# Performance work log

Measured on AMD Instinct MI355X. Metric: run time of the kernel, lower is better.

Reference implementation:

```python
import jax, jax.numpy as jnp
import numpy as np

V, E, H = 32000, 128, 128

def setup_inputs() -> dict:
    key = jax.random.key(0)
    ks = jax.random.split(key, 12)
    s = 0.05
    x = jax.random.randint(ks[0], (256, 512), 0, V)
    emb = jax.random.normal(ks[1], (V, E), jnp.float32) * s
    Wi = jax.random.normal(ks[2], (E + H, H), jnp.float32) * s
    bi = jnp.zeros((H,), jnp.float32)
    Wf = jax.random.normal(ks[3], (E + H, H), jnp.float32) * s
    bf = jnp.zeros((H,), jnp.float32)
    Wc = jax.random.normal(ks[4], (E + H, H), jnp.float32) * s
    bc = jnp.zeros((H,), jnp.float32)
    Wo = jax.random.normal(ks[5], (E + H, H), jnp.float32) * s
    bo = jnp.zeros((H,), jnp.float32)
    Wout = jax.random.normal(ks[6], (H, V), jnp.float32) * s
    bout = jnp.zeros((V,), jnp.float32)
    return {"x": x, "emb": emb, "Wi": Wi, "bi": bi, "Wf": Wf, "bf": bf,
            "Wc": Wc, "bc": bc, "Wo": Wo, "bo": bo, "Wout": Wout, "bout": bout}

def reference(x, emb, Wi, bi, Wf, bf, Wc, bc, Wo, bo, Wout, bout):
    B, T = x.shape
    xe = emb[x]                       # [B, T, E] embedding gather
    xe_t = jnp.swapaxes(xe, 0, 1)     # [T, B, E] for scan over time

    def step(carry, e_t):
        h, c = carry
        comb = jnp.concatenate([e_t, h], axis=1)          # [B, E+H]
        f = jax.nn.sigmoid(comb @ Wf + bf)
        i = jax.nn.sigmoid(comb @ Wi + bi)
        o = jax.nn.sigmoid(comb @ Wo + bo)
        c_ = jnp.tanh(comb @ Wc + bc)
        c = f * c + i * c_
        h = o * jnp.tanh(c)
        return (h, c), None

    h0 = jnp.zeros((B, H), xe.dtype)
    c0 = jnp.zeros((B, H), xe.dtype)
    (h, _), _ = jax.lax.scan(step, (h0, c0), xe_t)
    return h @ Wout + bout            # [B, V] logits from final hidden state
```

## Files before the change

kernel.cpp:

```cpp
#include <hip/hip_runtime.h>

constexpr int TT = 512;
constexpr int BB = 256;
constexpr int HH = 128;
constexpr int VV = 32000;

typedef _Float16 h2 __attribute__((ext_vector_type(2)));
typedef _Float16 f16x4 __attribute__((ext_vector_type(4)));
typedef _Float16 f16x8 __attribute__((ext_vector_type(8)));
typedef float f32x4 __attribute__((ext_vector_type(4)));

struct __align__(16) H2x4 { h2 a, b, c, d; };

__device__ __forceinline__ h2 pkrtz(float a, float b) {
  return __builtin_bit_cast(h2, __builtin_amdgcn_cvt_pkrtz(a, b));
}
__device__ __forceinline__ float fexp2(float x) {
  return __builtin_amdgcn_exp2f(x);
}
__device__ __forceinline__ float frcp(float x) {
  return __builtin_amdgcn_rcpf(x);
}
__device__ __forceinline__ float fdot2(h2 a, h2 b, float c) {
  return __builtin_amdgcn_fdot2(a, b, c, false);
}
template <int CTRL>
__device__ __forceinline__ float qmov(float v) {
  return __builtin_bit_cast(
      float, __builtin_amdgcn_mov_dpp(__builtin_bit_cast(int, v), CTRL, 0xf,
                                      0xf, true));
}

constexpr float SC_SIG = -1.4426950408889634f;
constexpr float SC_TANH = 2.8853900817779268f;

__global__ __launch_bounds__(256, 4) void wprep(
    const float* __restrict__ Wi, const float* __restrict__ bi,
    const float* __restrict__ Wf, const float* __restrict__ bf,
    const float* __restrict__ Wc, const float* __restrict__ bc,
    const float* __restrict__ Wo, const float* __restrict__ bo,
    _Float16* __restrict__ Wct, float* __restrict__ bcat) {
  const int n = blockIdx.x;
  const int g = n & 3;
  const int u = n >> 2;
  const float* Wg = (g == 0) ? Wi : (g == 1) ? Wf : (g == 2) ? Wc : Wo;
  const float* bg = (g == 0) ? bi : (g == 1) ? bf : (g == 2) ? bc : bo;
  const float sc = (g == 2) ? SC_TANH : SC_SIG;
  const int k = threadIdx.x;
  Wct[(size_t)n * 256 + k] = (_Float16)(Wg[(size_t)k * HH + u] * sc);
  if (k == 0) bcat[n] = bg[u] * sc;
}

__global__ __launch_bounds__(512, 2) void lstm_rec(
    const int* __restrict__ x, const float* __restrict__ emb,
    const _Float16* __restrict__ Wct, const float* __restrict__ bcat,
    _Float16* __restrict__ hbf) {
  const int b = blockIdx.x;
  const int tid = threadIdx.x;
  const int g = tid & 3;
  const int u = tid >> 2;
  const int w = tid >> 6;
  const int l = tid & 63;
  const int n16 = l & 15;
  const int quad = l >> 4;

  __shared__ int xrow[TT];
  __shared__ __align__(16) _Float16 comb[2][HH];
  __shared__ __align__(16) _Float16 xch[64][516];

  xrow[tid] = x[(size_t)b * TT + tid];
  if (tid < HH) comb[0][tid] = (_Float16)0.f;

  h2 wh2[64];
  {
    const _Float16* wp = Wct + (size_t)tid * 256 + 128;
#pragma unroll
    for (int j = 0; j < 16; ++j) {
      const H2x4 q = __builtin_bit_cast(H2x4, *(const f16x8*)(wp + 8 * j));
      wh2[4 * j + 0] = q.a;
      wh2[4 * j + 1] = q.b;
      wh2[4 * j + 2] = q.c;
      wh2[4 * j + 3] = q.d;
    }
  }

  f16x8 wfx[4][4];
  f32x4 biasr[4];
#pragma unroll
  for (int nt = 0; nt < 4; ++nt) {
#pragma unroll
    for (int ks = 0; ks < 4; ++ks)
      wfx[nt][ks] = *(const f16x8*)(Wct +
                                    (size_t)(64 * w + nt * 16 + n16) * 256 +
                                    ks * 32 + quad * 8);
    biasr[nt] = *(const f32x4*)(bcat + 64 * w + nt * 16 + quad * 4);
  }

  const float gam = (g == 2) ? -2.f : 1.f;
  const float del = (g == 2) ? 1.f : 0.f;

  const f32x4 ZR4 = {0.f, 0.f, 0.f, 0.f};

  float cst = 0.f;
  float hv = 0.f;
  int buf = 0;

  __syncthreads();

  for (int c = 0; c < 8; ++c) {
#pragma unroll 2
    for (int tt = 0; tt < 4; ++tt) {
      const int vid = xrow[c * 64 + tt * 16 + n16];
      const float* ep = emb + (size_t)vid * HH + quad * 8;
      f16x8 ef[4];
#pragma unroll
      for (int ks = 0; ks < 4; ++ks) {
        const float4 e0 = *(const float4*)(ep + ks * 32);
        const float4 e1 = *(const float4*)(ep + ks * 32 + 4);
        H2x4 q;
        q.a = pkrtz(e0.x, e0.y);
        q.b = pkrtz(e0.z, e0.w);
        q.c = pkrtz(e1.x, e1.y);
        q.d = pkrtz(e1.z, e1.w);
        ef[ks] = __builtin_bit_cast(f16x8, q);
      }
      f32x4 acc[4];
#pragma unroll
      for (int nt = 0; nt < 4; ++nt)
        acc[nt] = __builtin_amdgcn_mfma_f32_16x16x32_f16(wfx[nt][0], ef[0],
                                                         ZR4, 0, 0, 0);
#pragma unroll
      for (int ks = 1; ks < 4; ++ks)
#pragma unroll
        for (int nt = 0; nt < 4; ++nt)
          acc[nt] = __builtin_amdgcn_mfma_f32_16x16x32_f16(wfx[nt][ks], ef[ks],
                                                           acc[nt], 0, 0, 0);
#pragma unroll
      for (int nt = 0; nt < 4; ++nt) {
        const f32x4 av = acc[nt] + biasr[nt];
        _Float16* dst = &xch[tt * 16 + n16][64 * w + nt * 16 + quad * 4];
        *(h2*)dst = pkrtz(av[0], av[1]);
        *(h2*)(dst + 2) = pkrtz(av[2], av[3]);
      }
    }
    __syncthreads();

#pragma unroll 2
    for (int tl = 0; tl < 64; ++tl) {
      const float xe = (float)xch[tl][tid];

      const _Float16* cb = comb[buf];
      float s0 = 0.f, s1 = 0.f, s2 = 0.f, s3 = 0.f;
#pragma unroll
      for (int j = 0; j < 16; ++j) {
        const H2x4 hq = __builtin_bit_cast(H2x4, *(const f16x8*)(cb + 8 * j));
        s0 = fdot2(hq.a, wh2[4 * j + 0], s0);
        s1 = fdot2(hq.b, wh2[4 * j + 1], s1);
        s2 = fdot2(hq.c, wh2[4 * j + 2], s2);
        s3 = fdot2(hq.d, wh2[4 * j + 3], s3);
      }
      const float a = (s0 + s1) + (s2 + s3) + xe;

      const float act = gam * frcp(1.f + fexp2(a)) + del;

      const float x1 = qmov<0xB1>(act);
      const float x2 = qmov<0x4E>(act);
      const float x3 = qmov<0x4E>(x1);

      cst = x1 * cst + act * x2;
      const float th = 1.f - 2.f * frcp(1.f + fexp2(cst * SC_TANH));
      hv = x3 * th;

      if (g == 0) comb[buf ^ 1][u] = (_Float16)hv;
      __syncthreads();
      buf ^= 1;
    }
  }
  if (g == 0) hbf[(size_t)b * HH + u] = (_Float16)hv;
}

__global__ __launch_bounds__(256, 4) void wout_tr(const float* __restrict__ Wout,
                                                  _Float16* __restrict__ Wt) {
  const int v = blockIdx.x * 256 + threadIdx.x;
#pragma unroll 1
  for (int kc = 0; kc < 16; ++kc) {
    float f[8];
#pragma unroll
    for (int i = 0; i < 8; ++i) f[i] = Wout[(size_t)(kc * 8 + i) * VV + v];
    H2x4 q;
    q.a = pkrtz(f[0], f[1]);
    q.b = pkrtz(f[2], f[3]);
    q.c = pkrtz(f[4], f[5]);
    q.d = pkrtz(f[6], f[7]);
    *(H2x4*)(Wt + (size_t)v * HH + kc * 8) = q;
  }
}

__global__ __launch_bounds__(256, 4) void lstm_out(
    const _Float16* __restrict__ Wt, const _Float16* __restrict__ hbf,
    const float* __restrict__ bout, float* __restrict__ out) {
  const int tid = threadIdx.x;
  const int wv = tid >> 6;
  const int lane = tid & 63;
  const int vblk = blockIdx.x % 250;
  const int batblk = blockIdx.x / 250;
  const int n16 = lane & 15;
  const int quad = lane >> 4;
  const int vbase = vblk * 128 + wv * 32;
  const int batbase = batblk * 64;

  f32x4 acc[4][2] = {};
#pragma unroll
  for (int ks = 0; ks < 4; ++ks) {
    const int k = ks * 32 + quad * 8;
    f16x8 a[4], bf_[2];
#pragma unroll
    for (int mt = 0; mt < 4; ++mt)
      a[mt] = *(const f16x8*)(hbf + (size_t)(batbase + mt * 16 + n16) * HH + k);
#pragma unroll
    for (int vt = 0; vt < 2; ++vt)
      bf_[vt] = *(const f16x8*)(Wt + (size_t)(vbase + vt * 16 + n16) * HH + k);
#pragma unroll
    for (int mt = 0; mt < 4; ++mt)
#pragma unroll
      for (int vt = 0; vt < 2; ++vt)
        acc[mt][vt] = __builtin_amdgcn_mfma_f32_16x16x32_f16(a[mt], bf_[vt],
                                                             acc[mt][vt], 0, 0, 0);
  }
#pragma unroll
  for (int vt = 0; vt < 2; ++vt) {
    const int v = vbase + vt * 16 + n16;
    const float bv = bout[v];
#pragma unroll
    for (int mt = 0; mt < 4; ++mt) {
#pragma unroll
      for (int r = 0; r < 4; ++r) {
        const int bat = batbase + mt * 16 + quad * 4 + r;
        out[(size_t)bat * VV + v] = acc[mt][vt][r] + bv;
      }
    }
  }
}

extern "C" void kernel_launch(void* const* d_in, const int* in_sizes, int n_in,
                              void* d_out, int out_size, void* d_ws,
                              size_t ws_size, hipStream_t stream) {
  const int* x = (const int*)d_in[0];
  const float* emb = (const float*)d_in[1];
  const float* Wi = (const float*)d_in[2];
  const float* bi = (const float*)d_in[3];
  const float* Wf = (const float*)d_in[4];
  const float* bf = (const float*)d_in[5];
  const float* Wc = (const float*)d_in[6];
  const float* bc = (const float*)d_in[7];
  const float* Wo = (const float*)d_in[8];
  const float* bo = (const float*)d_in[9];
  const float* Wout = (const float*)d_in[10];
  const float* bout = (const float*)d_in[11];
  float* out = (float*)d_out;

  _Float16* Wt = (_Float16*)d_ws;
  _Float16* hbf = Wt + (size_t)VV * HH;
  _Float16* Wct = hbf + (size_t)BB * HH;
  float* bcat = (float*)(Wct + 512 * 256);

  wprep<<<512, 256, 0, stream>>>(Wi, bi, Wf, bf, Wc, bc, Wo, bo, Wct, bcat);
  wout_tr<<<VV / 256, 256, 0, stream>>>(Wout, Wt);
  lstm_rec<<<BB, 512, 0, stream>>>(x, emb, Wct, bcat, hbf);
  lstm_out<<<(VV / 128) * (BB / 64), 256, 0, stream>>>(Wt, hbf, bout, out);
}
```

Measured before the change: 439.7 us.

## Split recurrent dot product across two lanes with 1024-thread blocks

Doubles the recurrence block to 1024 threads, so each gate row's hidden-state dot product is split over two lanes (64 elements each) and combined with a ds_swizzle xor-4 exchange. The input-projection MFMA weights are no longer kept in registers; they are loaded from global memory on each tile, and each wave now handles 32 gate rows instead of 64. This halves the serial fdot2 chain and the weight registers per thread, shortening the per-timestep critical path. In exchange it adds a cross-lane swizzle and a 1024-thread barrier on every step, plus repeated global weight loads in the projection phase.

```diff
diff --git a/kernel.cpp b/kernel.cpp
--- a/kernel.cpp
+++ b/kernel.cpp
@@ -29,6 +29,10 @@
   return __builtin_bit_cast(
       float, __builtin_amdgcn_mov_dpp(__builtin_bit_cast(int, v), CTRL, 0xf,
                                       0xf, true));
+}
+__device__ __forceinline__ float swz_xor4(float v) {
+  return __builtin_bit_cast(
+      float, __builtin_amdgcn_ds_swizzle(__builtin_bit_cast(int, v), 0x101F));
 }
 
 constexpr float SC_SIG = -1.4426950408889634f;
@@ -51,31 +55,34 @@
   if (k == 0) bcat[n] = bg[u] * sc;
 }
 
-__global__ __launch_bounds__(512, 2) void lstm_rec(
+__global__ __launch_bounds__(1024, 4) void lstm_rec(
     const int* __restrict__ x, const float* __restrict__ emb,
     const _Float16* __restrict__ Wct, const float* __restrict__ bcat,
     _Float16* __restrict__ hbf) {
   const int b = blockIdx.x;
   const int tid = threadIdx.x;
-  const int g = tid & 3;
-  const int u = tid >> 2;
   const int w = tid >> 6;
   const int l = tid & 63;
   const int n16 = l & 15;
   const int quad = l >> 4;
+  const int g = l & 3;
+  const int kh = (l >> 2) & 1;
+  const int uloc = l >> 3;
+  const int u = 8 * w + uloc;
+  const int n = 32 * w + 4 * uloc + g;
 
   __shared__ int xrow[TT];
   __shared__ __align__(16) _Float16 comb[2][HH];
   __shared__ __align__(16) _Float16 xch[64][516];
 
-  xrow[tid] = x[(size_t)b * TT + tid];
+  if (tid < TT) xrow[tid] = x[(size_t)b * TT + tid];
   if (tid < HH) comb[0][tid] = (_Float16)0.f;
 
-  h2 wh2[64];
+  h2 wh2[32];
   {
-    const _Float16* wp = Wct + (size_t)tid * 256 + 128;
-#pragma unroll
-    for (int j = 0; j < 16; ++j) {
+    const _Float16* wp = Wct + (size_t)n * 256 + 128 + 64 * kh;
+#pragma unroll
+    for (int j = 0; j < 8; ++j) {
       const H2x4 q = __builtin_bit_cast(H2x4, *(const f16x8*)(wp + 8 * j));
       wh2[4 * j + 0] = q.a;
       wh2[4 * j + 1] = q.b;
@@ -84,18 +91,6 @@
     }
   }
 
-  f16x8 wfx[4][4];
-  f32x4 biasr[4];
-#pragma unroll
-  for (int nt = 0; nt < 4; ++nt) {
-#pragma unroll
-    for (int ks = 0; ks < 4; ++ks)
-      wfx[nt][ks] = *(const f16x8*)(Wct +
-                                    (size_t)(64 * w + nt * 16 + n16) * 256 +
-                                    ks * 32 + quad * 8);
-    biasr[nt] = *(const f32x4*)(bcat + 64 * w + nt * 16 + quad * 4);
-  }
-
   const float gam = (g == 2) ? -2.f : 1.f;
   const float del = (g == 2) ? 1.f : 0.f;
 
@@ -108,7 +103,7 @@
   __syncthreads();
 
   for (int c = 0; c < 8; ++c) {
-#pragma unroll 2
+#pragma unroll 1
     for (int tt = 0; tt < 4; ++tt) {
       const int vid = xrow[c * 64 + tt * 16 + n16];
       const float* ep = emb + (size_t)vid * HH + quad * 8;
@@ -124,21 +119,19 @@
         q.d = pkrtz(e1.z, e1.w);
         ef[ks] = __builtin_bit_cast(f16x8, q);
       }
-      f32x4 acc[4];
-#pragma unroll
-      for (int nt = 0; nt < 4; ++nt)
-        acc[nt] = __builtin_amdgcn_mfma_f32_16x16x32_f16(wfx[nt][0], ef[0],
-                                                         ZR4, 0, 0, 0);
-#pragma unroll
-      for (int ks = 1; ks < 4; ++ks)
-#pragma unroll
-        for (int nt = 0; nt < 4; ++nt)
-          acc[nt] = __builtin_amdgcn_mfma_f32_16x16x32_f16(wfx[nt][ks], ef[ks],
-                                                           acc[nt], 0, 0, 0);
-#pragma unroll
-      for (int nt = 0; nt < 4; ++nt) {
-        const f32x4 av = acc[nt] + biasr[nt];
-        _Float16* dst = &xch[tt * 16 + n16][64 * w + nt * 16 + quad * 4];
+#pragma unroll
+      for (int nt = 0; nt < 2; ++nt) {
+        const _Float16* wbase = Wct + (size_t)(32 * w + nt * 16 + n16) * 256;
+        f32x4 acc = __builtin_amdgcn_mfma_f32_16x16x32_f16(
+            *(const f16x8*)(wbase + 0 * 32 + quad * 8), ef[0], ZR4, 0, 0, 0);
+#pragma unroll
+        for (int ks = 1; ks < 4; ++ks)
+          acc = __builtin_amdgcn_mfma_f32_16x16x32_f16(
+              *(const f16x8*)(wbase + ks * 32 + quad * 8), ef[ks], acc, 0, 0,
+              0);
+        const f32x4 av =
+            acc + *(const f32x4*)(bcat + 32 * w + nt * 16 + quad * 4);
+        _Float16* dst = &xch[tt * 16 + n16][32 * w + nt * 16 + quad * 4];
         *(h2*)dst = pkrtz(av[0], av[1]);
         *(h2*)(dst + 2) = pkrtz(av[2], av[3]);
       }
@@ -147,19 +140,20 @@
 
 #pragma unroll 2
     for (int tl = 0; tl < 64; ++tl) {
-      const float xe = (float)xch[tl][tid];
-
-      const _Float16* cb = comb[buf];
+      const float xe = (float)xch[tl][n];
+
+      const _Float16* cb = &comb[buf][64 * kh];
       float s0 = 0.f, s1 = 0.f, s2 = 0.f, s3 = 0.f;
 #pragma unroll
-      for (int j = 0; j < 16; ++j) {
+      for (int j = 0; j < 8; ++j) {
         const H2x4 hq = __builtin_bit_cast(H2x4, *(const f16x8*)(cb + 8 * j));
         s0 = fdot2(hq.a, wh2[4 * j + 0], s0);
         s1 = fdot2(hq.b, wh2[4 * j + 1], s1);
         s2 = fdot2(hq.c, wh2[4 * j + 2], s2);
         s3 = fdot2(hq.d, wh2[4 * j + 3], s3);
       }
-      const float a = (s0 + s1) + (s2 + s3) + xe;
+      const float sh = (s0 + s1) + (s2 + s3);
+      const float a = sh + swz_xor4(sh) + xe;
 
       const float act = gam * frcp(1.f + fexp2(a)) + del;
 
@@ -171,12 +165,12 @@
       const float th = 1.f - 2.f * frcp(1.f + fexp2(cst * SC_TANH));
       hv = x3 * th;
 
-      if (g == 0) comb[buf ^ 1][u] = (_Float16)hv;
+      if ((l & 7) == 0) comb[buf ^ 1][u] = (_Float16)hv;
       __syncthreads();
       buf ^= 1;
     }
   }
-  if (g == 0) hbf[(size_t)b * HH + u] = (_Float16)hv;
+  if ((l & 7) == 0) hbf[(size_t)b * HH + u] = (_Float16)hv;
 }
 
 __global__ __launch_bounds__(256, 4) void wout_tr(const float* __restrict__ Wout,
@@ -266,6 +260,6 @@
 
   wprep<<<512, 256, 0, stream>>>(Wi, bi, Wf, bf, Wc, bc, Wo, bo, Wct, bcat);
   wout_tr<<<VV / 256, 256, 0, stream>>>(Wout, Wt);
-  lstm_rec<<<BB, 512, 0, stream>>>(x, emb, Wct, bcat, hbf);
+  lstm_rec<<<BB, 1024, 0, stream>>>(x, emb, Wct, bcat, hbf);
   lstm_out<<<(VV / 128) * (BB / 64), 256, 0, stream>>>(Wt, hbf, bout, out);
 }
```

Result: slower. 541.8 us (+23.2%).

## Split recurrent matvec between packed dot2 lanes and MFMA per step

Applied to the files above, without the earlier changes.

Per timestep, each wave's 64 gate rows are now split. The first 32 rows are computed with packed fp16 dot2, with each row's 128-element reduction divided across two lanes and combined by a cross-lane shuffle. The other 32 rows are computed with 16x16x32 MFMAs on the broadcast hidden state, and their results pass through a small LDS buffer. The aim is to halve the serial dot2 chain on the recurrence critical path and lower weight register use. The MFMA tiles waste most of their columns and add an LDS write/read inside the latency-bound step. Separately, the input-projection bias is now folded into the MFMA accumulator initialisation.

```diff
diff --git a/kernel.cpp b/kernel.cpp
--- a/kernel.cpp
+++ b/kernel.cpp
@@ -57,32 +57,44 @@
     _Float16* __restrict__ hbf) {
   const int b = blockIdx.x;
   const int tid = threadIdx.x;
-  const int g = tid & 3;
-  const int u = tid >> 2;
   const int w = tid >> 6;
   const int l = tid & 63;
   const int n16 = l & 15;
   const int quad = l >> 4;
+  const int g = l & 3;
+  const int u = 16 * w + (l >> 2);
+  const int drow = 64 * w + (l & 31);
+  const int khalf = l >> 5;
 
   __shared__ int xrow[TT];
   __shared__ __align__(16) _Float16 comb[2][HH];
   __shared__ __align__(16) _Float16 xch[64][516];
+  __shared__ __align__(16) float pre[8][32];
 
   xrow[tid] = x[(size_t)b * TT + tid];
   if (tid < HH) comb[0][tid] = (_Float16)0.f;
 
-  h2 wh2[64];
+  h2 wd[32];
   {
-    const _Float16* wp = Wct + (size_t)tid * 256 + 128;
-#pragma unroll
-    for (int j = 0; j < 16; ++j) {
+    const _Float16* wp = Wct + (size_t)drow * 256 + 128 + 64 * khalf;
+#pragma unroll
+    for (int j = 0; j < 8; ++j) {
       const H2x4 q = __builtin_bit_cast(H2x4, *(const f16x8*)(wp + 8 * j));
-      wh2[4 * j + 0] = q.a;
-      wh2[4 * j + 1] = q.b;
-      wh2[4 * j + 2] = q.c;
-      wh2[4 * j + 3] = q.d;
+      wd[4 * j + 0] = q.a;
+      wd[4 * j + 1] = q.b;
+      wd[4 * j + 2] = q.c;
+      wd[4 * j + 3] = q.d;
     }
   }
+
+  f16x8 whm[2][4];
+#pragma unroll
+  for (int nt = 0; nt < 2; ++nt)
+#pragma unroll
+    for (int ks = 0; ks < 4; ++ks)
+      whm[nt][ks] =
+          *(const f16x8*)(Wct + (size_t)(64 * w + 32 + nt * 16 + n16) * 256 +
+                          128 + ks * 32 + quad * 8);
 
   f16x8 wfx[4][4];
   f32x4 biasr[4];
@@ -98,8 +110,6 @@
 
   const float gam = (g == 2) ? -2.f : 1.f;
   const float del = (g == 2) ? 1.f : 0.f;
-
-  const f32x4 ZR4 = {0.f, 0.f, 0.f, 0.f};
 
   float cst = 0.f;
   float hv = 0.f;
@@ -128,7 +138,7 @@
 #pragma unroll
       for (int nt = 0; nt < 4; ++nt)
         acc[nt] = __builtin_amdgcn_mfma_f32_16x16x32_f16(wfx[nt][0], ef[0],
-                                                         ZR4, 0, 0, 0);
+                                                         biasr[nt], 0, 0, 0);
 #pragma unroll
       for (int ks = 1; ks < 4; ++ks)
 #pragma unroll
@@ -137,10 +147,9 @@
                                                            acc[nt], 0, 0, 0);
 #pragma unroll
       for (int nt = 0; nt < 4; ++nt) {
-        const f32x4 av = acc[nt] + biasr[nt];
         _Float16* dst = &xch[tt * 16 + n16][64 * w + nt * 16 + quad * 4];
-        *(h2*)dst = pkrtz(av[0], av[1]);
-        *(h2*)(dst + 2) = pkrtz(av[2], av[3]);
+        *(h2*)dst = pkrtz(acc[nt][0], acc[nt][1]);
+        *(h2*)(dst + 2) = pkrtz(acc[nt][2], acc[nt][3]);
       }
     }
     __syncthreads();
@@ -150,16 +159,47 @@
       const float xe = (float)xch[tl][tid];
 
       const _Float16* cb = comb[buf];
+
+      const _Float16* cd = cb + 64 * khalf;
       float s0 = 0.f, s1 = 0.f, s2 = 0.f, s3 = 0.f;
 #pragma unroll
-      for (int j = 0; j < 16; ++j) {
-        const H2x4 hq = __builtin_bit_cast(H2x4, *(const f16x8*)(cb + 8 * j));
-        s0 = fdot2(hq.a, wh2[4 * j + 0], s0);
-        s1 = fdot2(hq.b, wh2[4 * j + 1], s1);
-        s2 = fdot2(hq.c, wh2[4 * j + 2], s2);
-        s3 = fdot2(hq.d, wh2[4 * j + 3], s3);
-      }
-      const float a = (s0 + s1) + (s2 + s3) + xe;
+      for (int j = 0; j < 8; ++j) {
+        const H2x4 hq = __builtin_bit_cast(H2x4, *(const f16x8*)(cd + 8 * j));
+        s0 = fdot2(hq.a, wd[4 * j + 0], s0);
+        s1 = fdot2(hq.b, wd[4 * j + 1], s1);
+        s2 = fdot2(hq.c, wd[4 * j + 2], s2);
+        s3 = fdot2(hq.d, wd[4 * j + 3], s3);
+      }
+      const float part = (s0 + s1) + (s2 + s3);
+
+      f16x8 hb[4];
+#pragma unroll
+      for (int ks = 0; ks < 4; ++ks)
+        hb[ks] = *(const f16x8*)(cb + ks * 32 + quad * 8);
+      f32x4 am0 = __builtin_amdgcn_mfma_f32_16x16x32_f16(whm[0][0], hb[0],
+                                                         f32x4{0.f, 0.f, 0.f, 0.f},
+                                                         0, 0, 0);
+      f32x4 am1 = __builtin_amdgcn_mfma_f32_16x16x32_f16(whm[1][0], hb[0],
+                                                         f32x4{0.f, 0.f, 0.f, 0.f},
+                                                         0, 0, 0);
+#pragma unroll
+      for (int ks = 1; ks < 4; ++ks) {
+        am0 = __builtin_amdgcn_mfma_f32_16x16x32_f16(whm[0][ks], hb[ks], am0,
+                                                     0, 0, 0);
+        am1 = __builtin_amdgcn_mfma_f32_16x16x32_f16(whm[1][ks], hb[ks], am1,
+                                                     0, 0, 0);
+      }
+      if (n16 == 0) {
+        *(f32x4*)&pre[w][4 * quad] = am0;
+        *(f32x4*)&pre[w][16 + 4 * quad] = am1;
+      }
+
+      const float full = part + __shfl_xor(part, 32);
+
+      float apre;
+      if (l < 32) apre = full;
+      else apre = pre[w][l - 32];
+      const float a = apre + xe;
 
       const float act = gam * frcp(1.f + fexp2(a)) + del;
 
```

Measured after the change: 481.5 us. 9.5% more time.

## Rotate hidden state across lanes via DPP instead of broadcast LDS reads

Applied to the files above, without the earlier changes.

In the recurrent step, each lane now loads one 16-byte slice of the hidden vector from LDS and rotates it across 16-lane rows with DPP row_ror, with the recurrent weights pre-permuted per lane to match. This replaces 16 broadcast LDS reads per step and is meant to shorten the latency-bound serial loop. The MFMA weight fragments are now reloaded per chunk inside a scope to lower register pressure, the bias is folded into the first MFMA accumulator, and the two prep kernels are merged into one launch. The risks are DPP latency on the dependency chain and repeated global weight reloads.

```diff
diff --git a/kernel.cpp b/kernel.cpp
--- a/kernel.cpp
+++ b/kernel.cpp
@@ -30,25 +30,48 @@
       float, __builtin_amdgcn_mov_dpp(__builtin_bit_cast(int, v), CTRL, 0xf,
                                       0xf, true));
 }
+__device__ __forceinline__ int ror1_i(int v) {
+  return __builtin_amdgcn_mov_dpp(v, 0x121, 0xf, 0xf, true);
+}
+__device__ __forceinline__ h2 ror1_h(h2 v) {
+  return __builtin_bit_cast(h2, ror1_i(__builtin_bit_cast(int, v)));
+}
 
 constexpr float SC_SIG = -1.4426950408889634f;
 constexpr float SC_TANH = 2.8853900817779268f;
 
-__global__ __launch_bounds__(256, 4) void wprep(
+__global__ __launch_bounds__(256, 4) void prep(
     const float* __restrict__ Wi, const float* __restrict__ bi,
     const float* __restrict__ Wf, const float* __restrict__ bf,
     const float* __restrict__ Wc, const float* __restrict__ bc,
     const float* __restrict__ Wo, const float* __restrict__ bo,
-    _Float16* __restrict__ Wct, float* __restrict__ bcat) {
-  const int n = blockIdx.x;
-  const int g = n & 3;
-  const int u = n >> 2;
-  const float* Wg = (g == 0) ? Wi : (g == 1) ? Wf : (g == 2) ? Wc : Wo;
-  const float* bg = (g == 0) ? bi : (g == 1) ? bf : (g == 2) ? bc : bo;
-  const float sc = (g == 2) ? SC_TANH : SC_SIG;
-  const int k = threadIdx.x;
-  Wct[(size_t)n * 256 + k] = (_Float16)(Wg[(size_t)k * HH + u] * sc);
-  if (k == 0) bcat[n] = bg[u] * sc;
+    _Float16* __restrict__ Wct, float* __restrict__ bcat,
+    const float* __restrict__ Wout, _Float16* __restrict__ Wt) {
+  if (blockIdx.x < 512) {
+    const int n = blockIdx.x;
+    const int g = n & 3;
+    const int u = n >> 2;
+    const float* Wg = (g == 0) ? Wi : (g == 1) ? Wf : (g == 2) ? Wc : Wo;
+    const float* bg = (g == 0) ? bi : (g == 1) ? bf : (g == 2) ? bc : bo;
+    const float sc = (g == 2) ? SC_TANH : SC_SIG;
+    const int k = threadIdx.x;
+    Wct[(size_t)n * 256 + k] = (_Float16)(Wg[(size_t)k * HH + u] * sc);
+    if (k == 0) bcat[n] = bg[u] * sc;
+  } else {
+    const int v = (blockIdx.x - 512) * 256 + threadIdx.x;
+#pragma unroll 1
+    for (int kc = 0; kc < 16; ++kc) {
+      float f[8];
+#pragma unroll
+      for (int i = 0; i < 8; ++i) f[i] = Wout[(size_t)(kc * 8 + i) * VV + v];
+      H2x4 q;
+      q.a = pkrtz(f[0], f[1]);
+      q.b = pkrtz(f[2], f[3]);
+      q.c = pkrtz(f[4], f[5]);
+      q.d = pkrtz(f[6], f[7]);
+      *(H2x4*)(Wt + (size_t)v * HH + kc * 8) = q;
+    }
+  }
 }
 
 __global__ __launch_bounds__(512, 2) void lstm_rec(
@@ -71,35 +94,25 @@
   xrow[tid] = x[(size_t)b * TT + tid];
   if (tid < HH) comb[0][tid] = (_Float16)0.f;
 
-  h2 wh2[64];
+  const int pv = ror1_i(n16);
+  const int dstep = (n16 - pv) & 15;
+
+  h2 wr[16][4];
   {
     const _Float16* wp = Wct + (size_t)tid * 256 + 128;
 #pragma unroll
-    for (int j = 0; j < 16; ++j) {
-      const H2x4 q = __builtin_bit_cast(H2x4, *(const f16x8*)(wp + 8 * j));
-      wh2[4 * j + 0] = q.a;
-      wh2[4 * j + 1] = q.b;
-      wh2[4 * j + 2] = q.c;
-      wh2[4 * j + 3] = q.d;
-    }
-  }
-
-  f16x8 wfx[4][4];
-  f32x4 biasr[4];
-#pragma unroll
-  for (int nt = 0; nt < 4; ++nt) {
-#pragma unroll
-    for (int ks = 0; ks < 4; ++ks)
-      wfx[nt][ks] = *(const f16x8*)(Wct +
-                                    (size_t)(64 * w + nt * 16 + n16) * 256 +
-                                    ks * 32 + quad * 8);
-    biasr[nt] = *(const f32x4*)(bcat + 64 * w + nt * 16 + quad * 4);
+    for (int r = 0; r < 16; ++r) {
+      const int cidx = (n16 - r * dstep) & 15;
+      const H2x4 q = __builtin_bit_cast(H2x4, *(const f16x8*)(wp + 8 * cidx));
+      wr[r][0] = q.a;
+      wr[r][1] = q.b;
+      wr[r][2] = q.c;
+      wr[r][3] = q.d;
+    }
   }
 
   const float gam = (g == 2) ? -2.f : 1.f;
   const float del = (g == 2) ? 1.f : 0.f;
-
-  const f32x4 ZR4 = {0.f, 0.f, 0.f, 0.f};
 
   float cst = 0.f;
   float hv = 0.f;
@@ -108,39 +121,51 @@
   __syncthreads();
 
   for (int c = 0; c < 8; ++c) {
+    {
+      f16x8 wfx[4][4];
+      f32x4 biasr[4];
+#pragma unroll
+      for (int nt = 0; nt < 4; ++nt) {
+#pragma unroll
+        for (int ks = 0; ks < 4; ++ks)
+          wfx[nt][ks] =
+              *(const f16x8*)(Wct + (size_t)(64 * w + nt * 16 + n16) * 256 +
+                              ks * 32 + quad * 8);
+        biasr[nt] = *(const f32x4*)(bcat + 64 * w + nt * 16 + quad * 4);
+      }
 #pragma unroll 2
-    for (int tt = 0; tt < 4; ++tt) {
-      const int vid = xrow[c * 64 + tt * 16 + n16];
-      const float* ep = emb + (size_t)vid * HH + quad * 8;
-      f16x8 ef[4];
-#pragma unroll
-      for (int ks = 0; ks < 4; ++ks) {
-        const float4 e0 = *(const float4*)(ep + ks * 32);
-        const float4 e1 = *(const float4*)(ep + ks * 32 + 4);
-        H2x4 q;
-        q.a = pkrtz(e0.x, e0.y);
-        q.b = pkrtz(e0.z, e0.w);
-        q.c = pkrtz(e1.x, e1.y);
-        q.d = pkrtz(e1.z, e1.w);
-        ef[ks] = __builtin_bit_cast(f16x8, q);
-      }
-      f32x4 acc[4];
-#pragma unroll
-      for (int nt = 0; nt < 4; ++nt)
-        acc[nt] = __builtin_amdgcn_mfma_f32_16x16x32_f16(wfx[nt][0], ef[0],
-                                                         ZR4, 0, 0, 0);
-#pragma unroll
-      for (int ks = 1; ks < 4; ++ks)
+      for (int tt = 0; tt < 4; ++tt) {
+        const int vid = xrow[c * 64 + tt * 16 + n16];
+        const float* ep = emb + (size_t)vid * HH + quad * 8;
+        f16x8 ef[4];
+#pragma unroll
+        for (int ks = 0; ks < 4; ++ks) {
+          const float4 e0 = *(const float4*)(ep + ks * 32);
+          const float4 e1 = *(const float4*)(ep + ks * 32 + 4);
+          H2x4 q;
+          q.a = pkrtz(e0.x, e0.y);
+          q.b = pkrtz(e0.z, e0.w);
+          q.c = pkrtz(e1.x, e1.y);
+          q.d = pkrtz(e1.z, e1.w);
+          ef[ks] = __builtin_bit_cast(f16x8, q);
+        }
+        f32x4 acc[4];
 #pragma unroll
         for (int nt = 0; nt < 4; ++nt)
-          acc[nt] = __builtin_amdgcn_mfma_f32_16x16x32_f16(wfx[nt][ks], ef[ks],
-                                                           acc[nt], 0, 0, 0);
-#pragma unroll
-      for (int nt = 0; nt < 4; ++nt) {
-        const f32x4 av = acc[nt] + biasr[nt];
-        _Float16* dst = &xch[tt * 16 + n16][64 * w + nt * 16 + quad * 4];
-        *(h2*)dst = pkrtz(av[0], av[1]);
-        *(h2*)(dst + 2) = pkrtz(av[2], av[3]);
+          acc[nt] = __builtin_amdgcn_mfma_f32_16x16x32_f16(wfx[nt][0], ef[0],
+                                                           biasr[nt], 0, 0, 0);
+#pragma unroll
+        for (int ks = 1; ks < 4; ++ks)
+#pragma unroll
+          for (int nt = 0; nt < 4; ++nt)
+            acc[nt] = __builtin_amdgcn_mfma_f32_16x16x32_f16(
+                wfx[nt][ks], ef[ks], acc[nt], 0, 0, 0);
+#pragma unroll
+        for (int nt = 0; nt < 4; ++nt) {
+          _Float16* dst = &xch[tt * 16 + n16][64 * w + nt * 16 + quad * 4];
+          *(h2*)dst = pkrtz(acc[nt][0], acc[nt][1]);
+          *(h2*)(dst + 2) = pkrtz(acc[nt][2], acc[nt][3]);
+        }
       }
     }
     __syncthreads();
@@ -149,15 +174,22 @@
     for (int tl = 0; tl < 64; ++tl) {
       const float xe = (float)xch[tl][tid];
 
-      const _Float16* cb = comb[buf];
+      H2x4 hq =
+          __builtin_bit_cast(H2x4, *(const f16x8*)(&comb[buf][8 * n16]));
+
       float s0 = 0.f, s1 = 0.f, s2 = 0.f, s3 = 0.f;
 #pragma unroll
-      for (int j = 0; j < 16; ++j) {
-        const H2x4 hq = __builtin_bit_cast(H2x4, *(const f16x8*)(cb + 8 * j));
-        s0 = fdot2(hq.a, wh2[4 * j + 0], s0);
-        s1 = fdot2(hq.b, wh2[4 * j + 1], s1);
-        s2 = fdot2(hq.c, wh2[4 * j + 2], s2);
-        s3 = fdot2(hq.d, wh2[4 * j + 3], s3);
+      for (int r = 0; r < 16; ++r) {
+        s0 = fdot2(hq.a, wr[r][0], s0);
+        s1 = fdot2(hq.b, wr[r][1], s1);
+        s2 = fdot2(hq.c, wr[r][2], s2);
+        s3 = fdot2(hq.d, wr[r][3], s3);
+        if (r < 15) {
+          hq.a = ror1_h(hq.a);
+          hq.b = ror1_h(hq.b);
+          hq.c = ror1_h(hq.c);
+          hq.d = ror1_h(hq.d);
+        }
       }
       const float a = (s0 + s1) + (s2 + s3) + xe;
 
@@ -177,23 +209,6 @@
     }
   }
   if (g == 0) hbf[(size_t)b * HH + u] = (_Float16)hv;
-}
-
-__global__ __launch_bounds__(256, 4) void wout_tr(const float* __restrict__ Wout,
-                                                  _Float16* __restrict__ Wt) {
-  const int v = blockIdx.x * 256 + threadIdx.x;
-#pragma unroll 1
-  for (int kc = 0; kc < 16; ++kc) {
-    float f[8];
-#pragma unroll
-    for (int i = 0; i < 8; ++i) f[i] = Wout[(size_t)(kc * 8 + i) * VV + v];
-    H2x4 q;
-    q.a = pkrtz(f[0], f[1]);
-    q.b = pkrtz(f[2], f[3]);
-    q.c = pkrtz(f[4], f[5]);
-    q.d = pkrtz(f[6], f[7]);
-    *(H2x4*)(Wt + (size_t)v * HH + kc * 8) = q;
-  }
 }
 
 __global__ __launch_bounds__(256, 4) void lstm_out(
@@ -264,8 +279,8 @@
   _Float16* Wct = hbf + (size_t)BB * HH;
   float* bcat = (float*)(Wct + 512 * 256);
 
-  wprep<<<512, 256, 0, stream>>>(Wi, bi, Wf, bf, Wc, bc, Wo, bo, Wct, bcat);
-  wout_tr<<<VV / 256, 256, 0, stream>>>(Wout, Wt);
+  prep<<<512 + VV / 256, 256, 0, stream>>>(Wi, bi, Wf, bf, Wc, bc, Wo, bo,
+                                           Wct, bcat, Wout, Wt);
   lstm_rec<<<BB, 512, 0, stream>>>(x, emb, Wct, bcat, hbf);
   lstm_out<<<(VV / 128) * (BB / 64), 256, 0, stream>>>(Wt, hbf, bout, out);
 }
```

Result: slower. 514.1 us (+16.9%).
